# Optimization experiments

Measured on AMD Instinct MI355X. Metric: run time of the kernel, lower is better.

## Reference

```python
import jax, jax.numpy as jnp
import numpy as np

N_NODES = 50000
N_EDGES = 800000
N_GRAPHS = 256
C_FEAT = 108
MLP_DIM = 88
OUT_DIM = 100


def setup_inputs() -> dict:
    key = jax.random.key(0)
    ks = jax.random.split(key, 12)
    x = jax.random.normal(ks[0], (N_NODES, C_FEAT), dtype=jnp.float32)
    edge_index = jax.random.randint(ks[1], (2, N_EDGES), 0, N_NODES, dtype=jnp.int64)
    batch = jnp.sort(jax.random.randint(ks[2], (N_NODES,), 0, N_GRAPHS, dtype=jnp.int64))

    def glorot(k, shape):
        fan_in, fan_out = shape
        s = jnp.sqrt(2.0 / (fan_in + fan_out))
        return jax.random.normal(k, shape, dtype=jnp.float32) * s

    return {
        "x": x,
        "edge_index": edge_index,
        "batch": batch,
        # SAGEConv layer 1: lin_l (neighbors, has bias), lin_r (root, no bias)
        "W1l": glorot(ks[3], (C_FEAT, MLP_DIM)),
        "W1r": glorot(ks[4], (C_FEAT, MLP_DIM)),
        "b1": jnp.zeros((MLP_DIM,), jnp.float32),
        "W2l": glorot(ks[5], (MLP_DIM, MLP_DIM)),
        "W2r": glorot(ks[6], (MLP_DIM, MLP_DIM)),
        "b2": jnp.zeros((MLP_DIM,), jnp.float32),
        "W3l": glorot(ks[7], (MLP_DIM, MLP_DIM)),
        "W3r": glorot(ks[8], (MLP_DIM, MLP_DIM)),
        "b3": jnp.zeros((MLP_DIM,), jnp.float32),
        "Wlin": glorot(ks[9], (MLP_DIM, OUT_DIM)),
        "blin": jnp.zeros((OUT_DIM,), jnp.float32),
    }


def _sage_conv(x, src, dst, Wl, Wr, b):
    """PyG SAGEConv(aggr='mean'): out = lin_l(mean_j x_j) + lin_r(x)."""
    n = x.shape[0]
    msg = x[src]  # [E, d] gather from source nodes
    agg = jax.ops.segment_sum(msg, dst, num_segments=n)  # [N, d]
    cnt = jax.ops.segment_sum(jnp.ones((src.shape[0],), x.dtype), dst, num_segments=n)
    agg = agg / jnp.maximum(cnt, 1.0)[:, None]  # scatter-mean
    return agg @ Wl + b + x @ Wr


def reference(x, edge_index, batch, W1l, W1r, b1, W2l, W2r, b2, W3l, W3r, b3, Wlin, blin):
    src, dst = edge_index[0], edge_index[1]
    h = jax.nn.relu(_sage_conv(x, src, dst, W1l, W1r, b1))
    h = jax.nn.relu(_sage_conv(h, src, dst, W2l, W2r, b2))
    h = jax.nn.relu(_sage_conv(h, src, dst, W3l, W3r, b3))
    pooled = jax.ops.segment_sum(h, batch, num_segments=N_GRAPHS)  # global_add_pool
    return pooled @ Wlin + blin  # [n_graphs, 100]
```

## Files before the change

kernel.cpp:

```cpp
#include <hip/hip_runtime.h>
#include <hip/hip_fp16.h>

#define NN 50000
#define NG 256
#define CF 108
#define MD 88
#define OD 100
#define F2 44
#define HP 96
#define HP2 48
#define YLS 96
#define K1P 128
#define NSB 196
#define SBCAP 5120
#define TILE 2048
#define NCH 12

typedef _Float16 f16x8 __attribute__((ext_vector_type(8)));
typedef float f32x4 __attribute__((ext_vector_type(4)));


__global__ __launch_bounds__(256) void bin_kernel(const int* __restrict__ edge, int E,
                                                  int* __restrict__ sbcur,
                                                  unsigned* __restrict__ sbrec) {
    __shared__ int bcnt[NSB], boff[NSB], bfill[NSB], gbase[NSB];
    __shared__ int sc[256];
    __shared__ unsigned stag[TILE];
    __shared__ unsigned char stagbin[TILE];
    const int tid = threadIdx.x;
    const int t0  = blockIdx.x * TILE;
    const int tcnt = min(TILE, E - t0);

    for (int i = tid; i < NSB; i += 256) bcnt[i] = 0;
    __syncthreads();

    unsigned recs[TILE / 256];
    int      bins[TILE / 256];
    #pragma unroll
    for (int j = 0; j < TILE / 256; ++j) {
        const int e = t0 + j * 256 + tid;
        bins[j] = -1;
        if (e < E) {
            const int dst = edge[E + e], src = edge[e];
            bins[j] = dst >> 8;
            recs[j] = ((unsigned)src << 8) | (unsigned)(dst & 255);
            atomicAdd(&bcnt[bins[j]], 1);
        }
    }
    __syncthreads();

    sc[tid] = (tid < NSB) ? bcnt[tid] : 0;
    __syncthreads();
    for (int d = 1; d < 256; d <<= 1) {
        int v = (tid >= d) ? sc[tid - d] : 0;
        __syncthreads();
        sc[tid] += v;
        __syncthreads();
    }
    if (tid < NSB) {
        boff[tid]  = sc[tid] - bcnt[tid];
        bfill[tid] = sc[tid] - bcnt[tid];
        if (bcnt[tid] > 0) gbase[tid] = atomicAdd(&sbcur[tid], bcnt[tid]);
    }
    __syncthreads();

    #pragma unroll
    for (int j = 0; j < TILE / 256; ++j) {
        if (bins[j] >= 0) {
            int pos = atomicAdd(&bfill[bins[j]], 1);
            stag[pos]    = recs[j];
            stagbin[pos] = (unsigned char)bins[j];
        }
    }
    __syncthreads();

    for (int i = tid; i < tcnt; i += 256) {
        const int b   = stagbin[i];
        const int rel = i - boff[b];
        const int gp  = gbase[b] + rel;
        if (gp < SBCAP) sbrec[(size_t)b * SBCAP + gp] = stag[i];
    }
}


__global__ __launch_bounds__(256) void csr256_kernel(const unsigned* __restrict__ sbrec,
                                                     const int* __restrict__ sbcur,
                                                     int* __restrict__ csr,
                                                     int2* __restrict__ off2, int N) {
    __shared__ int hist[256], base[256], offc[256], sc[256];
    const int b = blockIdx.x, tid = threadIdx.x;
    const int cnt = min(sbcur[b], SBCAP);
    const unsigned* rec = sbrec + (size_t)b * SBCAP;

    hist[tid] = 0;
    __syncthreads();
    for (int r = tid; r < cnt; r += 256) atomicAdd(&hist[rec[r] & 255u], 1);
    __syncthreads();

    sc[tid] = hist[tid];
    __syncthreads();
    for (int d = 1; d < 256; d <<= 1) {
        int v = (tid >= d) ? sc[tid - d] : 0;
        __syncthreads();
        sc[tid] += v;
        __syncthreads();
    }
    base[tid] = sc[tid] - hist[tid];
    offc[tid] = base[tid];
    __syncthreads();

    for (int r = tid; r < cnt; r += 256) {
        const unsigned u = rec[r];
        const int dl = (int)(u & 255u);
        const int pos = atomicAdd(&offc[dl], 1);
        csr[(size_t)b * SBCAP + pos] = (int)(u >> 8);
    }
    __syncthreads();

    const int n = b * 256 + tid;
    if (n < N) off2[n] = make_int2(b * SBCAP + base[tid], hist[tid]);
}


__global__ void convx_kernel(const float* __restrict__ x, _Float16* __restrict__ xh, int N) {
    int i = blockIdx.x * blockDim.x + threadIdx.x;
    if (i >= N * K1P) return;
    int n = i >> 7, k = i & (K1P - 1);
    xh[i] = (k < CF) ? (_Float16)x[n * CF + k] : (_Float16)0.f;
}


__global__ void build_wct_all(const float* __restrict__ W1l, const float* __restrict__ W1r,
                              const float* __restrict__ W2l, const float* __restrict__ W2r,
                              const float* __restrict__ W3l, const float* __restrict__ W3r,
                              _Float16* __restrict__ Wct1, _Float16* __restrict__ Wct23) {
    const int n1 = 176 * K1P;
    const int n2 = 176 * HP;
    int idx = blockIdx.x * blockDim.x + threadIdx.x;
    if (idx < n1) {
        int c = idx / K1P, k = idx - c * K1P;
        float v = (k < CF) ? ((c < MD) ? W1l[k * MD + c] : W1r[k * MD + (c - MD)]) : 0.f;
        Wct1[idx] = (_Float16)v;
    } else if (idx < n1 + 2 * n2) {
        int j = idx - n1;
        const float* Wl = (j < n2) ? W2l : W3l;
        const float* Wr = (j < n2) ? W2r : W3r;
        int jj = (j < n2) ? j : j - n2;
        int c = jj / HP, k = jj - c * HP;
        float v = (k < MD) ? ((c < MD) ? Wl[k * MD + c] : Wr[k * MD + (c - MD)]) : 0.f;
        Wct23[j] = (_Float16)v;
    }
}


template <int KPAD>
__global__ __launch_bounds__(256) void gemm_mfma_kernel(const _Float16* __restrict__ Ah,
                                                        const _Float16* __restrict__ Wct,
                                                        const float* __restrict__ bias,
                                                        _Float16* __restrict__ yl,
                                                        _Float16* __restrict__ yr, int N) {
    const int wave = threadIdx.x >> 6;
    const int lane = threadIdx.x & 63;
    const int r16  = lane & 15;
    const int kg   = lane >> 4;
    const int rbase = blockIdx.x * 64 + wave * 16;

    const int arow = min(rbase + r16, N - 1);
    const _Float16* ap = Ah + (size_t)arow * KPAD + kg * 8;

    f32x4 acc[11];
    #pragma unroll
    for (int t = 0; t < 11; ++t) acc[t] = (f32x4){0.f, 0.f, 0.f, 0.f};

    #pragma unroll
    for (int ks = 0; ks < KPAD / 32; ++ks) {
        f16x8 af = *(const f16x8*)(ap + ks * 32);
        #pragma unroll
        for (int t = 0; t < 11; ++t) {
            const _Float16* bp = Wct + (size_t)(t * 16 + r16) * KPAD + ks * 32 + kg * 8;
            f16x8 bf = *(const f16x8*)bp;
            acc[t] = __builtin_amdgcn_mfma_f32_16x16x32_f16(af, bf, acc[t], 0, 0, 0);
        }
    }

    const int orow0 = rbase + kg * 4;
    #pragma unroll
    for (int t = 0; t < 11; ++t) {
        const int c = t * 16 + r16;
        const bool isr = (c >= MD);
        const float bv = isr ? bias[c - MD] : 0.f;
        _Float16* dst = isr ? (yr + (c - MD)) : (yl + c);
        const int st = isr ? MD : YLS;
        #pragma unroll
        for (int r = 0; r < 4; ++r) {
            const int row = orow0 + r;
            if (row < N) dst[(size_t)row * st] = (_Float16)(acc[t][r] + bv);
        }
    }
}


__global__ void agg_kernel(const _Float16* __restrict__ yl, const _Float16* __restrict__ yr,
                           const int2* __restrict__ off2, const int* __restrict__ csr,
                           _Float16* __restrict__ h, int N) {
    int idx = blockIdx.x * blockDim.x + threadIdx.x;
    if (idx >= N * NCH) return;
    int n = idx / NCH;
    int c = idx - n * NCH;
    if (c >= 11) {
        *(f16x8*)(h + (size_t)n * HP + 88) = (f16x8)(_Float16)0.f;
        return;
    }
    const int2 o = off2[n];
    const int s = o.x, e = o.x + o.y;
    float a0[8] = {0,0,0,0,0,0,0,0}, a1[8] = {0,0,0,0,0,0,0,0};
    float a2[8] = {0,0,0,0,0,0,0,0}, a3[8] = {0,0,0,0,0,0,0,0};
    const size_t cof = (size_t)c * 8;
    int i = s;
    for (; i + 3 < e; i += 4) {
        f16x8 v0 = *(const f16x8*)(yl + (size_t)csr[i]     * YLS + cof);
        f16x8 v1 = *(const f16x8*)(yl + (size_t)csr[i + 1] * YLS + cof);
        f16x8 v2 = *(const f16x8*)(yl + (size_t)csr[i + 2] * YLS + cof);
        f16x8 v3 = *(const f16x8*)(yl + (size_t)csr[i + 3] * YLS + cof);
        #pragma unroll
        for (int j = 0; j < 8; ++j) {
            a0[j] += (float)v0[j]; a1[j] += (float)v1[j];
            a2[j] += (float)v2[j]; a3[j] += (float)v3[j];
        }
    }
    for (; i < e; ++i) {
        f16x8 v0 = *(const f16x8*)(yl + (size_t)csr[i] * YLS + cof);
        #pragma unroll
        for (int j = 0; j < 8; ++j) a0[j] += (float)v0[j];
    }
    const float inv = 1.0f / (float)max(o.y, 1);
    const f16x8 r = *(const f16x8*)(yr + (size_t)n * MD + cof);
    f16x8 outv;
    #pragma unroll
    for (int j = 0; j < 8; ++j) {
        float v = (a0[j] + a1[j] + a2[j] + a3[j]) * inv + (float)r[j];
        outv[j] = (_Float16)fmaxf(v, 0.f);
    }
    *(f16x8*)(h + (size_t)n * HP + cof) = outv;
}


__global__ void gstarts_kernel(const int* __restrict__ batch, int* __restrict__ gstart, int n) {
    int i = blockIdx.x * blockDim.x + threadIdx.x;
    if (i >= n) return;
    int b = batch[i];
    int prev = (i == 0) ? -1 : batch[i - 1];
    for (int g = prev + 1; g <= b; ++g) gstart[g] = i;
    if (i == n - 1) {
        for (int g = b + 1; g <= NG; ++g) gstart[g] = n;
    }
}

__global__ __launch_bounds__(256) void pool_kernel(const __half2* __restrict__ h2,
                                                   const int* __restrict__ gstart,
                                                   float* __restrict__ pooled) {
    __shared__ float red[4][F2][2];
    const int g    = blockIdx.x;
    const int w    = threadIdx.x >> 6;
    const int lane = threadIdx.x & 63;
    const int s = gstart[g], e = gstart[g + 1];

    float ax0 = 0.f, ay0 = 0.f, ax1 = 0.f, ay1 = 0.f;
    if (lane < F2) {
        int n = s + w;
        for (; n + 4 < e; n += 8) {
            __half2 v0 = h2[(size_t)n * HP2 + lane];
            __half2 v1 = h2[(size_t)(n + 4) * HP2 + lane];
            ax0 += __low2float(v0); ay0 += __high2float(v0);
            ax1 += __low2float(v1); ay1 += __high2float(v1);
        }
        if (n < e) {
            __half2 v0 = h2[(size_t)n * HP2 + lane];
            ax0 += __low2float(v0); ay0 += __high2float(v0);
        }
        red[w][lane][0] = ax0 + ax1;
        red[w][lane][1] = ay0 + ay1;
    }
    __syncthreads();
    if (threadIdx.x < F2) {
        const int fp = threadIdx.x;
        float sx = red[0][fp][0] + red[1][fp][0] + red[2][fp][0] + red[3][fp][0];
        float sy = red[0][fp][1] + red[1][fp][1] + red[2][fp][1] + red[3][fp][1];
        float2* pp = (float2*)(pooled + (size_t)g * MD);
        pp[fp] = make_float2(sx, sy);
    }
}

__global__ void final_kernel(const float* __restrict__ pooled, const float* __restrict__ Wlin,
                             const float* __restrict__ blin, float* __restrict__ out) {
    int idx = blockIdx.x * blockDim.x + threadIdx.x;
    if (idx >= NG * OD) return;
    int g = idx / OD, o = idx - (idx / OD) * OD;
    float acc = blin[o];
    for (int f = 0; f < MD; ++f)
        acc = fmaf(pooled[g * MD + f], Wlin[f * OD + o], acc);
    out[idx] = acc;
}


extern "C" void kernel_launch(void* const* d_in, const int* in_sizes, int n_in,
                              void* d_out, int out_size, void* d_ws, size_t ws_size,
                              hipStream_t stream) {
    const float* x     = (const float*)d_in[0];
    const int*   edge  = (const int*)d_in[1];
    const int*   batch = (const int*)d_in[2];
    const float* W1l = (const float*)d_in[3];
    const float* W1r = (const float*)d_in[4];
    const float* b1  = (const float*)d_in[5];
    const float* W2l = (const float*)d_in[6];
    const float* W2r = (const float*)d_in[7];
    const float* b2  = (const float*)d_in[8];
    const float* W3l = (const float*)d_in[9];
    const float* W3r = (const float*)d_in[10];
    const float* b3  = (const float*)d_in[11];
    const float* Wlin = (const float*)d_in[12];
    const float* blin = (const float*)d_in[13];
    float* out = (float*)d_out;

    const int N = in_sizes[0] / CF;
    const int E = in_sizes[1] / 2;

    char* ws = (char*)d_ws;
    auto alloc = [&](size_t bytes) -> void* {
        void* p = (void*)ws;
        ws += (bytes + 255) & ~(size_t)255;
        return p;
    };
    int*       sbcur   = (int*)alloc((size_t)NSB * 4);
    unsigned*  sbrec   = (unsigned*)alloc((size_t)NSB * SBCAP * 4);
    int*       csr     = (int*)alloc((size_t)NSB * SBCAP * 4);
    int2*      off2    = (int2*)alloc((size_t)N * 8);
    int*       gstart  = (int*)alloc((size_t)(NG + 1) * 4);
    _Float16*  Wct1    = (_Float16*)alloc((size_t)176 * K1P * 2);
    _Float16*  Wct23   = (_Float16*)alloc((size_t)2 * 176 * HP * 2);
    _Float16*  xh      = (_Float16*)alloc((size_t)N * K1P * 2);
    _Float16*  yl      = (_Float16*)alloc((size_t)N * YLS * 2);
    _Float16*  yr      = (_Float16*)alloc((size_t)N * MD * 2);
    _Float16*  h       = (_Float16*)alloc((size_t)N * HP * 2);
    float*     pooled  = (float*)alloc((size_t)NG * MD * 4);

    hipMemsetAsync(sbcur, 0, (size_t)NSB * 4, stream);
    bin_kernel<<<(E + TILE - 1) / TILE, 256, 0, stream>>>(edge, E, sbcur, sbrec);
    csr256_kernel<<<NSB, 256, 0, stream>>>(sbrec, sbcur, csr, off2, N);

    convx_kernel<<<(N * K1P + 255) / 256, 256, 0, stream>>>(x, xh, N);
    build_wct_all<<<(176 * K1P + 2 * 176 * HP + 255) / 256, 256, 0, stream>>>(
        W1l, W1r, W2l, W2r, W3l, W3r, Wct1, Wct23);
    gstarts_kernel<<<(N + 255) / 256, 256, 0, stream>>>(batch, gstart, N);

    const int gemm_blocks = (N + 63) / 64;
    const int agg_blocks  = (N * NCH + 255) / 256;

    gemm_mfma_kernel<K1P><<<gemm_blocks, 256, 0, stream>>>(xh, Wct1, b1, yl, yr, N);
    agg_kernel<<<agg_blocks, 256, 0, stream>>>(yl, yr, off2, csr, h, N);

    gemm_mfma_kernel<HP><<<gemm_blocks, 256, 0, stream>>>(h, Wct23, b2, yl, yr, N);
    agg_kernel<<<agg_blocks, 256, 0, stream>>>(yl, yr, off2, csr, h, N);

    gemm_mfma_kernel<HP><<<gemm_blocks, 256, 0, stream>>>(h, Wct23 + (size_t)176 * HP, b3, yl, yr, N);
    agg_kernel<<<agg_blocks, 256, 0, stream>>>(yl, yr, off2, csr, h, N);

    pool_kernel<<<NG, 256, 0, stream>>>((const __half2*)h, gstart, pooled);
    final_kernel<<<(NG * OD + 255) / 256, 256, 0, stream>>>(pooled, Wlin, blin, out);
}
```

Measured before the change: 215.5 us.

## Double GEMM rows per wave, unroll gather by 8, fuse pool with final linear

The MFMA GEMM now has each wave compute two 16-row tiles, so every B fragment load is reused for two MFMAs and the grid is halved. The aggregation loop is unrolled to 8 neighbors with a 2-wide tail to keep more gathers in flight. The gstarts, pool and final kernels are merged into one kernel that binary-searches the sorted batch array for graph bounds and applies the output linear layer in shared memory, which removes two launches and the pooled buffer. The larger GEMM tile raises register pressure and halves the number of blocks, which may lower occupancy.

```diff
diff --git a/kernel.cpp b/kernel.cpp
--- a/kernel.cpp
+++ b/kernel.cpp
@@ -163,38 +163,47 @@
     const int lane = threadIdx.x & 63;
     const int r16  = lane & 15;
     const int kg   = lane >> 4;
-    const int rbase = blockIdx.x * 64 + wave * 16;
-
-    const int arow = min(rbase + r16, N - 1);
-    const _Float16* ap = Ah + (size_t)arow * KPAD + kg * 8;
-
-    f32x4 acc[11];
-    #pragma unroll
-    for (int t = 0; t < 11; ++t) acc[t] = (f32x4){0.f, 0.f, 0.f, 0.f};
+    const int rbase = blockIdx.x * 128 + wave * 16;
+
+    const int arow0 = min(rbase + r16, N - 1);
+    const int arow1 = min(rbase + 64 + r16, N - 1);
+    const _Float16* ap0 = Ah + (size_t)arow0 * KPAD + kg * 8;
+    const _Float16* ap1 = Ah + (size_t)arow1 * KPAD + kg * 8;
+
+    f32x4 acc[2][11];
+    #pragma unroll
+    for (int q = 0; q < 2; ++q)
+        #pragma unroll
+        for (int t = 0; t < 11; ++t) acc[q][t] = (f32x4){0.f, 0.f, 0.f, 0.f};
 
     #pragma unroll
     for (int ks = 0; ks < KPAD / 32; ++ks) {
-        f16x8 af = *(const f16x8*)(ap + ks * 32);
+        f16x8 af0 = *(const f16x8*)(ap0 + ks * 32);
+        f16x8 af1 = *(const f16x8*)(ap1 + ks * 32);
         #pragma unroll
         for (int t = 0; t < 11; ++t) {
             const _Float16* bp = Wct + (size_t)(t * 16 + r16) * KPAD + ks * 32 + kg * 8;
             f16x8 bf = *(const f16x8*)bp;
-            acc[t] = __builtin_amdgcn_mfma_f32_16x16x32_f16(af, bf, acc[t], 0, 0, 0);
-        }
-    }
-
-    const int orow0 = rbase + kg * 4;
-    #pragma unroll
-    for (int t = 0; t < 11; ++t) {
-        const int c = t * 16 + r16;
-        const bool isr = (c >= MD);
-        const float bv = isr ? bias[c - MD] : 0.f;
-        _Float16* dst = isr ? (yr + (c - MD)) : (yl + c);
-        const int st = isr ? MD : YLS;
-        #pragma unroll
-        for (int r = 0; r < 4; ++r) {
-            const int row = orow0 + r;
-            if (row < N) dst[(size_t)row * st] = (_Float16)(acc[t][r] + bv);
+            acc[0][t] = __builtin_amdgcn_mfma_f32_16x16x32_f16(af0, bf, acc[0][t], 0, 0, 0);
+            acc[1][t] = __builtin_amdgcn_mfma_f32_16x16x32_f16(af1, bf, acc[1][t], 0, 0, 0);
+        }
+    }
+
+    #pragma unroll
+    for (int q = 0; q < 2; ++q) {
+        const int orow0 = rbase + q * 64 + kg * 4;
+        #pragma unroll
+        for (int t = 0; t < 11; ++t) {
+            const int c = t * 16 + r16;
+            const bool isr = (c >= MD);
+            const float bv = isr ? bias[c - MD] : 0.f;
+            _Float16* dst = isr ? (yr + (c - MD)) : (yl + c);
+            const int st = isr ? MD : YLS;
+            #pragma unroll
+            for (int r = 0; r < 4; ++r) {
+                const int row = orow0 + r;
+                if (row < N) dst[(size_t)row * st] = (_Float16)(acc[q][t][r] + bv);
+            }
         }
     }
 }
@@ -217,18 +226,33 @@
     float a2[8] = {0,0,0,0,0,0,0,0}, a3[8] = {0,0,0,0,0,0,0,0};
     const size_t cof = (size_t)c * 8;
     int i = s;
-    for (; i + 3 < e; i += 4) {
+    for (; i + 7 < e; i += 8) {
         f16x8 v0 = *(const f16x8*)(yl + (size_t)csr[i]     * YLS + cof);
         f16x8 v1 = *(const f16x8*)(yl + (size_t)csr[i + 1] * YLS + cof);
         f16x8 v2 = *(const f16x8*)(yl + (size_t)csr[i + 2] * YLS + cof);
         f16x8 v3 = *(const f16x8*)(yl + (size_t)csr[i + 3] * YLS + cof);
+        f16x8 v4 = *(const f16x8*)(yl + (size_t)csr[i + 4] * YLS + cof);
+        f16x8 v5 = *(const f16x8*)(yl + (size_t)csr[i + 5] * YLS + cof);
+        f16x8 v6 = *(const f16x8*)(yl + (size_t)csr[i + 6] * YLS + cof);
+        f16x8 v7 = *(const f16x8*)(yl + (size_t)csr[i + 7] * YLS + cof);
         #pragma unroll
         for (int j = 0; j < 8; ++j) {
-            a0[j] += (float)v0[j]; a1[j] += (float)v1[j];
-            a2[j] += (float)v2[j]; a3[j] += (float)v3[j];
-        }
-    }
-    for (; i < e; ++i) {
+            a0[j] += (float)v0[j] + (float)v1[j];
+            a1[j] += (float)v2[j] + (float)v3[j];
+            a2[j] += (float)v4[j] + (float)v5[j];
+            a3[j] += (float)v6[j] + (float)v7[j];
+        }
+    }
+    for (; i + 1 < e; i += 2) {
+        f16x8 v0 = *(const f16x8*)(yl + (size_t)csr[i]     * YLS + cof);
+        f16x8 v1 = *(const f16x8*)(yl + (size_t)csr[i + 1] * YLS + cof);
+        #pragma unroll
+        for (int j = 0; j < 8; ++j) {
+            a0[j] += (float)v0[j];
+            a1[j] += (float)v1[j];
+        }
+    }
+    if (i < e) {
         f16x8 v0 = *(const f16x8*)(yl + (size_t)csr[i] * YLS + cof);
         #pragma unroll
         for (int j = 0; j < 8; ++j) a0[j] += (float)v0[j];
@@ -245,25 +269,30 @@
 }
 
 
-__global__ void gstarts_kernel(const int* __restrict__ batch, int* __restrict__ gstart, int n) {
-    int i = blockIdx.x * blockDim.x + threadIdx.x;
-    if (i >= n) return;
-    int b = batch[i];
-    int prev = (i == 0) ? -1 : batch[i - 1];
-    for (int g = prev + 1; g <= b; ++g) gstart[g] = i;
-    if (i == n - 1) {
-        for (int g = b + 1; g <= NG; ++g) gstart[g] = n;
-    }
-}
-
-__global__ __launch_bounds__(256) void pool_kernel(const __half2* __restrict__ h2,
-                                                   const int* __restrict__ gstart,
-                                                   float* __restrict__ pooled) {
+__global__ __launch_bounds__(256) void pool_final_kernel(const __half2* __restrict__ h2,
+                                                         const int* __restrict__ batch,
+                                                         const float* __restrict__ Wlin,
+                                                         const float* __restrict__ blin,
+                                                         float* __restrict__ out, int N) {
     __shared__ float red[4][F2][2];
+    __shared__ float pooled[MD];
+    __shared__ int range[2];
     const int g    = blockIdx.x;
-    const int w    = threadIdx.x >> 6;
-    const int lane = threadIdx.x & 63;
-    const int s = gstart[g], e = gstart[g + 1];
+    const int tid  = threadIdx.x;
+    const int w    = tid >> 6;
+    const int lane = tid & 63;
+
+    if (tid < 2) {
+        const int tgt = g + tid;
+        int lo = 0, hi = N;
+        while (lo < hi) {
+            int mid = (lo + hi) >> 1;
+            if (batch[mid] < tgt) lo = mid + 1; else hi = mid;
+        }
+        range[tid] = lo;
+    }
+    __syncthreads();
+    const int s = range[0], e = range[1];
 
     float ax0 = 0.f, ay0 = 0.f, ax1 = 0.f, ay1 = 0.f;
     if (lane < F2) {
@@ -282,24 +311,18 @@
         red[w][lane][1] = ay0 + ay1;
     }
     __syncthreads();
-    if (threadIdx.x < F2) {
-        const int fp = threadIdx.x;
-        float sx = red[0][fp][0] + red[1][fp][0] + red[2][fp][0] + red[3][fp][0];
-        float sy = red[0][fp][1] + red[1][fp][1] + red[2][fp][1] + red[3][fp][1];
-        float2* pp = (float2*)(pooled + (size_t)g * MD);
-        pp[fp] = make_float2(sx, sy);
-    }
-}
-
-__global__ void final_kernel(const float* __restrict__ pooled, const float* __restrict__ Wlin,
-                             const float* __restrict__ blin, float* __restrict__ out) {
-    int idx = blockIdx.x * blockDim.x + threadIdx.x;
-    if (idx >= NG * OD) return;
-    int g = idx / OD, o = idx - (idx / OD) * OD;
-    float acc = blin[o];
-    for (int f = 0; f < MD; ++f)
-        acc = fmaf(pooled[g * MD + f], Wlin[f * OD + o], acc);
-    out[idx] = acc;
+    if (tid < F2) {
+        pooled[2 * tid]     = red[0][tid][0] + red[1][tid][0] + red[2][tid][0] + red[3][tid][0];
+        pooled[2 * tid + 1] = red[0][tid][1] + red[1][tid][1] + red[2][tid][1] + red[3][tid][1];
+    }
+    __syncthreads();
+    if (tid < OD) {
+        float acc = blin[tid];
+        #pragma unroll 8
+        for (int f = 0; f < MD; ++f)
+            acc = fmaf(pooled[f], Wlin[f * OD + tid], acc);
+        out[(size_t)g * OD + tid] = acc;
+    }
 }
 
 
@@ -335,14 +358,12 @@
     unsigned*  sbrec   = (unsigned*)alloc((size_t)NSB * SBCAP * 4);
     int*       csr     = (int*)alloc((size_t)NSB * SBCAP * 4);
     int2*      off2    = (int2*)alloc((size_t)N * 8);
-    int*       gstart  = (int*)alloc((size_t)(NG + 1) * 4);
     _Float16*  Wct1    = (_Float16*)alloc((size_t)176 * K1P * 2);
     _Float16*  Wct23   = (_Float16*)alloc((size_t)2 * 176 * HP * 2);
     _Float16*  xh      = (_Float16*)alloc((size_t)N * K1P * 2);
     _Float16*  yl      = (_Float16*)alloc((size_t)N * YLS * 2);
     _Float16*  yr      = (_Float16*)alloc((size_t)N * MD * 2);
     _Float16*  h       = (_Float16*)alloc((size_t)N * HP * 2);
-    float*     pooled  = (float*)alloc((size_t)NG * MD * 4);
 
     hipMemsetAsync(sbcur, 0, (size_t)NSB * 4, stream);
     bin_kernel<<<(E + TILE - 1) / TILE, 256, 0, stream>>>(edge, E, sbcur, sbrec);
@@ -351,9 +372,8 @@
     convx_kernel<<<(N * K1P + 255) / 256, 256, 0, stream>>>(x, xh, N);
     build_wct_all<<<(176 * K1P + 2 * 176 * HP + 255) / 256, 256, 0, stream>>>(
         W1l, W1r, W2l, W2r, W3l, W3r, Wct1, Wct23);
-    gstarts_kernel<<<(N + 255) / 256, 256, 0, stream>>>(batch, gstart, N);
-
-    const int gemm_blocks = (N + 63) / 64;
+
+    const int gemm_blocks = (N + 127) / 128;
     const int agg_blocks  = (N * NCH + 255) / 256;
 
     gemm_mfma_kernel<K1P><<<gemm_blocks, 256, 0, stream>>>(xh, Wct1, b1, yl, yr, N);
@@ -365,6 +385,5 @@
     gemm_mfma_kernel<HP><<<gemm_blocks, 256, 0, stream>>>(h, Wct23 + (size_t)176 * HP, b3, yl, yr, N);
     agg_kernel<<<agg_blocks, 256, 0, stream>>>(yl, yr, off2, csr, h, N);
 
-    pool_kernel<<<NG, 256, 0, stream>>>((const __half2*)h, gstart, pooled);
-    final_kernel<<<(NG * OD + 255) / 256, 256, 0, stream>>>(pooled, Wlin, blin, out);
-}
+    pool_final_kernel<<<NG, 256, 0, stream>>>((const __half2*)h, batch, Wlin, blin, out, N);
+}
```

New measurement: 209.4 us. -2.8%, faster.
